# Kernel tuning notes

Hardware: AMD Instinct MI355X
Metric: run time of the kernel (lower is better)

## Reference

```python
import jax, jax.numpy as jnp
import numpy as np

X_CH, Y_CH, DIM, NUM_HEAD = 256, 512, 128, 4
H_DIM = DIM // NUM_HEAD
GAMMA = H_DIM ** (-0.5)


def conv1x1(x, w, b):
    # x: [B,C,H,W], w: [O,C], b: [O]
    return jnp.einsum('bchw,oc->bohw', x, w) + b[None, :, None, None]


def _split_qkv(qkv, bs, hw):
    # qkv: [B, 3*DIM, H, W] -> q,k,v each [B, NUM_HEAD, HW, H_DIM]
    qkv = qkv.reshape(bs, 3, NUM_HEAD, H_DIM, hw)
    qkv = jnp.transpose(qkv, (1, 0, 2, 4, 3))  # [3, B, H, HW, D]
    return qkv[0], qkv[1], qkv[2]


def setup_inputs() -> dict:
    key = jax.random.key(0)
    ks = jax.random.split(key, 12)
    s = lambda fan_in: 1.0 / np.sqrt(fan_in)
    x = jax.random.normal(ks[0], (2, X_CH, 64, 64), dtype=jnp.float32)
    y = jax.random.normal(ks[1], (2, Y_CH, 32, 32), dtype=jnp.float32)
    wx_qkv = jax.random.normal(ks[2], (3 * DIM, X_CH), dtype=jnp.float32) * s(X_CH)
    bx_qkv = jax.random.normal(ks[3], (3 * DIM,), dtype=jnp.float32) * s(X_CH)
    wy_qkv = jax.random.normal(ks[4], (3 * DIM, Y_CH), dtype=jnp.float32) * s(Y_CH)
    by_qkv = jax.random.normal(ks[5], (3 * DIM,), dtype=jnp.float32) * s(Y_CH)
    wpx = jax.random.normal(ks[6], (X_CH, DIM), dtype=jnp.float32) * s(DIM)
    bpx = jax.random.normal(ks[7], (X_CH,), dtype=jnp.float32) * s(DIM)
    wpy = jax.random.normal(ks[8], (Y_CH, DIM), dtype=jnp.float32) * s(DIM)
    bpy = jax.random.normal(ks[9], (Y_CH,), dtype=jnp.float32) * s(DIM)
    return {"x": x, "y": y, "wx_qkv": wx_qkv, "bx_qkv": bx_qkv,
            "wy_qkv": wy_qkv, "by_qkv": by_qkv,
            "wpx": wpx, "bpx": bpx, "wpy": wpy, "bpy": bpy}


def reference(x, y, wx_qkv, bx_qkv, wy_qkv, by_qkv, wpx, bpx, wpy, bpy):
    bs, _, h_x, w_x = x.shape
    _, _, h_y, w_y = y.shape
    hw_x, hw_y = h_x * w_x, h_y * w_y

    q_x, k_x, v_x = _split_qkv(conv1x1(x, wx_qkv, bx_qkv), bs, hw_x)
    q_y, k_y, v_y = _split_qkv(conv1x1(y, wy_qkv, by_qkv), bs, hw_y)

    # x attends to y
    atten_x = jax.nn.softmax(jnp.einsum('bhqd,bhkd->bhqk', q_x, k_y) * GAMMA, axis=-1)
    out_x = jnp.einsum('bhqk,bhkd->bhqd', atten_x, v_y)  # [B,H,HWx,D]
    out_x = jnp.transpose(out_x, (0, 1, 3, 2)).reshape(bs, DIM, h_x, w_x)

    # y attends to x
    atten_y = jax.nn.softmax(jnp.einsum('bhqd,bhkd->bhqk', q_y, k_x) * GAMMA, axis=-1)
    out_y = jnp.einsum('bhqk,bhkd->bhqd', atten_y, v_x)
    out_y = jnp.transpose(out_y, (0, 1, 3, 2)).reshape(bs, DIM, h_y, w_y)

    out_x = conv1x1(out_x, wpx, bpx) + x
    out_y = conv1x1(out_y, wpy, bpy) + y
    return out_x, out_y
```

## Files before the change

### kernel.cpp

```cpp
#include <hip/hip_runtime.h>
#include <hip/hip_bf16.h>
#include <cstdint>

#define B 2
#define NH 4
#define HD 32
#define DIM 128
#define CX 256
#define CY 512
#define PX 4096
#define PY 1024
#define QKV 384
#define GAMMA 0.17677669529663687f

typedef unsigned short u16;
typedef unsigned int u32;

using short8 = __attribute__((ext_vector_type(8))) short;
using f32x4  = __attribute__((ext_vector_type(4))) float;

__device__ __forceinline__ float bf2f(u32 h) {
  union { u32 u; float f; } v; v.u = (h & 0xffffu) << 16; return v.f;
}
__device__ __forceinline__ u16 f2bf(float f) {
  u32 u = __float_as_uint(f);
  u32 r = (u + 0x7fffu + ((u >> 16) & 1u)) >> 16;
  return (u16)r;
}
__device__ __forceinline__ bool is_f32(const void* src) {
  u32 u = ((const u16*)src)[2 * (threadIdx.x & 63)];
  return __ballot((u & 0x7F80u) >= 0x4600u) != 0ull;
}

#define N_X   (B * CX * PX)
#define N_Y   (B * CY * PY)
#define N_WX  (QKV * CX)
#define N_BX  (QKV)
#define N_WY  (QKV * CY)
#define N_BY  (QKV)
#define N_WPX (CX * DIM)
#define N_BPX (CX)
#define N_WPY (CY * DIM)
#define N_BPY (CY)

enum : size_t {
  OFF_CWX   = 0,
  OFF_CBX   = OFF_CWX  + N_WX,
  OFF_CWY   = OFF_CBX  + N_BX,
  OFF_CBY   = OFF_CWY  + N_WY,
  OFF_CWPX  = OFF_CBY  + N_BY,
  OFF_CBPX  = OFF_CWPX + N_WPX,
  OFF_CWPY  = OFF_CBPX + N_BPX,
  OFF_CBPY  = OFF_CWPY + N_WPY,
  OFF_XT    = OFF_CBPY + N_BPY,
  OFF_YT    = OFF_XT   + (size_t)B * PX * CX,
  OFF_QPX   = OFF_YT   + (size_t)B * PY * CY,
  OFF_KPX   = OFF_QPX  + (size_t)B * NH * PX * HD,
  OFF_QPY   = OFF_KPX  + (size_t)B * NH * PX * HD,
  OFF_KPY   = OFF_QPY  + (size_t)B * NH * PY * HD,
  OFF_VCX   = OFF_KPY  + (size_t)B * NH * PY * HD,
  OFF_VCY   = OFF_VCX  + (size_t)B * DIM * PX,
  OFF_OTX   = OFF_VCY  + (size_t)B * DIM * PY,
  OFF_OTY   = OFF_OTX  + (size_t)B * PX * DIM,
  WS_END    = OFF_OTY  + (size_t)B * PY * DIM,
};

#define XPX_BLKS 512
#define XPY_BLKS 256
__global__ __launch_bounds__(256) void k_prep(
    const void* x, const void* y, const void* wx, const void* bx,
    const void* wy, const void* by, const void* wpx, const void* bpx,
    const void* wpy, const void* bpy, u16* __restrict__ ws) {
  const int id = blockIdx.x;
  if (id < XPX_BLKS + XPY_BLKS) {
    __shared__ u16 tile[64][68];
    const void* src; u16* dst; int C, P, p_t, c_t, b;
    if (id < XPX_BLKS) {
      src = x; dst = ws + OFF_XT; C = CX; P = PX;
      p_t = id & 63; c_t = (id >> 6) & 3; b = id >> 8;
    } else {
      int id2 = id - XPX_BLKS;
      src = y; dst = ws + OFF_YT; C = CY; P = PY;
      p_t = id2 & 15; c_t = (id2 >> 4) & 7; b = id2 >> 7;
    }
    const bool f32in = is_f32(src);
    const int tx = threadIdx.x & 15, tc = threadIdx.x >> 4;
    const int p0 = p_t * 64, c0 = c_t * 64;
#pragma unroll
    for (int i = 0; i < 4; i++) {
      int cl = tc + i * 16;
      size_t sidx = ((size_t)b * C + c0 + cl) * P + p0 + tx * 4;
      u16 v0, v1, v2, v3;
      if (f32in) {
        float4 f = *(const float4*)((const float*)src + sidx);
        v0 = f2bf(f.x); v1 = f2bf(f.y); v2 = f2bf(f.z); v3 = f2bf(f.w);
      } else {
        uint2 u = *(const uint2*)((const u16*)src + sidx);
        v0 = (u16)u.x; v1 = (u16)(u.x >> 16); v2 = (u16)u.y; v3 = (u16)(u.y >> 16);
      }
      tile[tx * 4 + 0][cl] = v0; tile[tx * 4 + 1][cl] = v1;
      tile[tx * 4 + 2][cl] = v2; tile[tx * 4 + 3][cl] = v3;
    }
    __syncthreads();
#pragma unroll
    for (int i = 0; i < 4; i++) {
      int pl = tc + i * 16;
      *(uint2*)&dst[((size_t)b * P + p0 + pl) * C + c0 + tx * 4] =
          *(const uint2*)&tile[pl][tx * 4];
    }
  } else {
    int wid = id - (XPX_BLKS + XPY_BLKS);
    const void* src; size_t dstoff; int n, base;
    if      (wid < 48)  { src = wx;  dstoff = OFF_CWX;  n = N_WX;  base = 0; }
    else if (wid < 49)  { src = bx;  dstoff = OFF_CBX;  n = N_BX;  base = 48; }
    else if (wid < 145) { src = wy;  dstoff = OFF_CWY;  n = N_WY;  base = 49; }
    else if (wid < 146) { src = by;  dstoff = OFF_CBY;  n = N_BY;  base = 145; }
    else if (wid < 162) { src = wpx; dstoff = OFF_CWPX; n = N_WPX; base = 146; }
    else if (wid < 163) { src = bpx; dstoff = OFF_CBPX; n = N_BPX; base = 162; }
    else if (wid < 195) { src = wpy; dstoff = OFF_CWPY; n = N_WPY; base = 163; }
    else                { src = bpy; dstoff = OFF_CBPY; n = N_BPY; base = 195; }
    const bool f32in = is_f32(src);
    int e0 = (wid - base) * 2048 + threadIdx.x * 8;
    if (e0 >= n) return;
    u16* dst = ws + dstoff + e0;
    if (f32in) {
      const float* s = (const float*)src + e0;
      float4 a = *(const float4*)s;
      float4 bq = *(const float4*)(s + 4);
      ushort4 o0, o1;
      o0.x = f2bf(a.x);  o0.y = f2bf(a.y);  o0.z = f2bf(a.z);  o0.w = f2bf(a.w);
      o1.x = f2bf(bq.x); o1.y = f2bf(bq.y); o1.z = f2bf(bq.z); o1.w = f2bf(bq.w);
      *(ushort4*)dst = o0;
      *(ushort4*)(dst + 4) = o1;
    } else {
      uint4 v = *(const uint4*)((const u16*)src + e0);
      *(uint4*)dst = v;
    }
  }
}

__global__ __launch_bounds__(256) void k_qkv(u16* __restrict__ ws) {
  const int t = threadIdx.x;
  const int lane = t & 63, w = t >> 6;
  const int ql = lane & 15, quad = lane >> 4;
  const int b = blockIdx.z;

  const u16 *W, *Xt, *bias; u16 *qp, *kp, *vc; int C, P, pxb;
  if (blockIdx.x < 64) {
    W = ws + OFF_CWX; Xt = ws + OFF_XT; bias = ws + OFF_CBX;
    qp = ws + OFF_QPX; kp = ws + OFF_KPX; vc = ws + OFF_VCX;
    C = CX; P = PX; pxb = blockIdx.x;
  } else {
    W = ws + OFF_CWY; Xt = ws + OFF_YT; bias = ws + OFF_CBY;
    qp = ws + OFF_QPY; kp = ws + OFF_KPY; vc = ws + OFF_VCY;
    C = CY; P = PY; pxb = blockIdx.x - 64;
  }
  const int p_w = pxb * 64 + (w & 1) * 32;
  const int o_w = blockIdx.y * 64 + (w >> 1) * 32;

  const u16* wr0 = W + (size_t)(o_w + ql) * C;
  const u16* wr1 = W + (size_t)(o_w + 16 + ql) * C;
  const u16* xr0 = Xt + ((size_t)b * P + p_w + ql) * C;
  const u16* xr1 = Xt + ((size_t)b * P + p_w + 16 + ql) * C;

  union U { uint4 u; short8 s; };
  f32x4 acc[2][2];
#pragma unroll
  for (int i = 0; i < 2; i++)
#pragma unroll
    for (int j = 0; j < 2; j++) acc[i][j] = (f32x4){0.f, 0.f, 0.f, 0.f};

  const bool isv = blockIdx.y >= 4;
  if (!isv) {
#pragma unroll 4
    for (int c0 = 0; c0 < C; c0 += 32) {
      int off = c0 + quad * 8;
      U a0, a1, b0, b1;
      a0.u = *(const uint4*)&wr0[off];
      a1.u = *(const uint4*)&wr1[off];
      b0.u = *(const uint4*)&xr0[off];
      b1.u = *(const uint4*)&xr1[off];
      acc[0][0] = __builtin_amdgcn_mfma_f32_16x16x32_bf16(a0.s, b0.s, acc[0][0], 0, 0, 0);
      acc[0][1] = __builtin_amdgcn_mfma_f32_16x16x32_bf16(a0.s, b1.s, acc[0][1], 0, 0, 0);
      acc[1][0] = __builtin_amdgcn_mfma_f32_16x16x32_bf16(a1.s, b0.s, acc[1][0], 0, 0, 0);
      acc[1][1] = __builtin_amdgcn_mfma_f32_16x16x32_bf16(a1.s, b1.s, acc[1][1], 0, 0, 0);
    }
  } else {
#pragma unroll 4
    for (int c0 = 0; c0 < C; c0 += 32) {
      int off = c0 + quad * 8;
      U a0, a1, b0, b1;
      a0.u = *(const uint4*)&wr0[off];
      a1.u = *(const uint4*)&wr1[off];
      b0.u = *(const uint4*)&xr0[off];
      b1.u = *(const uint4*)&xr1[off];
      acc[0][0] = __builtin_amdgcn_mfma_f32_16x16x32_bf16(b0.s, a0.s, acc[0][0], 0, 0, 0);
      acc[0][1] = __builtin_amdgcn_mfma_f32_16x16x32_bf16(b1.s, a0.s, acc[0][1], 0, 0, 0);
      acc[1][0] = __builtin_amdgcn_mfma_f32_16x16x32_bf16(b0.s, a1.s, acc[1][0], 0, 0, 0);
      acc[1][1] = __builtin_amdgcn_mfma_f32_16x16x32_bf16(b1.s, a1.s, acc[1][1], 0, 0, 0);
    }
  }

  if (!isv) {
    float bs[2][4];
#pragma unroll
    for (int oi = 0; oi < 2; oi++)
#pragma unroll
      for (int r = 0; r < 4; r++)
        bs[oi][r] = bf2f(bias[o_w + oi * 16 + quad * 4 + r]);
    bool isq = blockIdx.y < 2;
    float scale = isq ? GAMMA : 1.0f;
    u16* dstT = isq ? qp : kp;
#pragma unroll
    for (int oi = 0; oi < 2; oi++)
#pragma unroll
      for (int pi = 0; pi < 2; pi++) {
        int p = p_w + pi * 16 + ql;
        int o = o_w + oi * 16 + quad * 4 - (isq ? 0 : 128);
        int hh = o >> 5, d = o & 31;
        f32x4 a = acc[oi][pi];
        uint2 pk;
        pk.x = (u32)f2bf((a[0] + bs[oi][0]) * scale) |
               ((u32)f2bf((a[1] + bs[oi][1]) * scale) << 16);
        pk.y = (u32)f2bf((a[2] + bs[oi][2]) * scale) |
               ((u32)f2bf((a[3] + bs[oi][3]) * scale) << 16);
        *(uint2*)&dstT[((size_t)(b * NH + hh) * P + p) * HD + d] = pk;
      }
  } else {
#pragma unroll
    for (int oi = 0; oi < 2; oi++) {
      int o = o_w + oi * 16 + ql - 256;
      float bv = bf2f(bias[o_w + oi * 16 + ql]);
#pragma unroll
      for (int pi = 0; pi < 2; pi++) {
        int pbase = p_w + pi * 16 + quad * 4;
        f32x4 a = acc[oi][pi];
        ushort4 st;
        st.x = f2bf(a[0] + bv); st.y = f2bf(a[1] + bv);
        st.z = f2bf(a[2] + bv); st.w = f2bf(a[3] + bv);
        *(ushort4*)&vc[((size_t)b * DIM + o) * P + pbase] = st;
      }
    }
  }
}

template <int NQF>
__device__ __forceinline__ void attn_core(
    const u16* __restrict__ Qp, const u16* __restrict__ Kp,
    const u16* __restrict__ Vc, u16* __restrict__ Ot, int Pq, int Pk,
    int q0, int h, int b, u16* pool, float (*lfb)[64]) {
  const int t = threadIdx.x;
  const int lane = t & 63, w = t >> 6;
  const int ql = lane & 15, quad = lane >> 4;

  union U { uint4 u; short8 s; };
  U qf[NQF];
#pragma unroll
  for (int qi = 0; qi < NQF; qi++)
    qf[qi].u = *(const uint4*)&Qp[((size_t)(b * NH + h) * Pq + q0 + qi * 16 + ql) * HD + quad * 8];

  const int kspan = Pk >> 2;
  const int kk0 = w * kspan;
  const int niter = kspan >> 5;
  const int f0 = ((ql >> 2) << 3) | (ql & 3);

  const u16* kbase = Kp + ((size_t)(b * NH + h) * Pk + kk0 + f0) * HD + quad * 8;
  const u16* v0base = Vc + ((size_t)(b * DIM + h * HD + ql)) * Pk + kk0 + quad * 8;
  const u16* v1base = v0base + (size_t)16 * Pk;

  U ka, kb, va, vb, kan, kbn, van, vbn;
  ka.u = *(const uint4*)&kbase[0];
  kb.u = *(const uint4*)&kbase[4 * HD];
  va.u = *(const uint4*)&v0base[0];
  vb.u = *(const uint4*)&v1base[0];

  f32x4 o0[NQF], o1[NQF];
  float l_run[NQF];
#pragma unroll
  for (int qi = 0; qi < NQF; qi++) {
    o0[qi] = (f32x4){0.f, 0.f, 0.f, 0.f};
    o1[qi] = (f32x4){0.f, 0.f, 0.f, 0.f};
    l_run[qi] = 0.f;
  }

  for (int it = 0; it < niter; it++) {
    if (it + 1 < niter) {
      size_t go = (size_t)(it + 1) * 32;
      kan.u = *(const uint4*)&kbase[go * HD];
      kbn.u = *(const uint4*)&kbase[(go + 4) * HD];
      van.u = *(const uint4*)&v0base[go];
      vbn.u = *(const uint4*)&v1base[go];
    }

#pragma unroll
    for (int qi = 0; qi < NQF; qi++) {
      f32x4 z = {0.f, 0.f, 0.f, 0.f};
      f32x4 st0 = __builtin_amdgcn_mfma_f32_16x16x32_bf16(ka.s, qf[qi].s, z, 0, 0, 0);
      f32x4 st1 = __builtin_amdgcn_mfma_f32_16x16x32_bf16(kb.s, qf[qi].s, z, 0, 0, 0);

      float p[8];
#pragma unroll
      for (int r = 0; r < 4; r++) { p[r] = __expf(st0[r]); p[4 + r] = __expf(st1[r]); }
      l_run[qi] += ((p[0] + p[1]) + (p[2] + p[3])) + ((p[4] + p[5]) + (p[6] + p[7]));

      U pf;
      pf.u.x = __builtin_amdgcn_perm(__float_as_uint(p[1]), __float_as_uint(p[0]), 0x07060302u);
      pf.u.y = __builtin_amdgcn_perm(__float_as_uint(p[3]), __float_as_uint(p[2]), 0x07060302u);
      pf.u.z = __builtin_amdgcn_perm(__float_as_uint(p[5]), __float_as_uint(p[4]), 0x07060302u);
      pf.u.w = __builtin_amdgcn_perm(__float_as_uint(p[7]), __float_as_uint(p[6]), 0x07060302u);

      o0[qi] = __builtin_amdgcn_mfma_f32_16x16x32_bf16(va.s, pf.s, o0[qi], 0, 0, 0);
      o1[qi] = __builtin_amdgcn_mfma_f32_16x16x32_bf16(vb.s, pf.s, o1[qi], 0, 0, 0);
    }
    ka = kan; kb = kbn; va = van; vb = vbn;
  }

#pragma unroll
  for (int qi = 0; qi < NQF; qi++) {
    float l = l_run[qi];
    l += __shfl_xor(l, 16);
    l += __shfl_xor(l, 32);
    l_run[qi] = l;
  }

  float* Of = (float*)(pool + (size_t)w * 4096);
#pragma unroll
  for (int qi = 0; qi < NQF; qi++) {
#pragma unroll
    for (int r = 0; r < 4; r++) {
      Of[(qi * 16 + ql) * 32 + quad * 4 + r] = o0[qi][r];
      Of[(qi * 16 + ql) * 32 + 16 + quad * 4 + r] = o1[qi][r];
    }
    if (quad == 0) lfb[w][qi * 16 + ql] = l_run[qi];
  }
  __syncthreads();

  const float* OfA = (const float*)pool;
#pragma unroll
  for (int k = 0; k < NQF * 2; k++) {
    int e = t + k * 256;
    int q = e >> 5, d = e & 31;
    float lt = lfb[0][q] + lfb[1][q] + lfb[2][q] + lfb[3][q];
    int di = q * 32 + d;
    float v = (OfA[di] + OfA[2048 + di]) + (OfA[4096 + di] + OfA[6144 + di]);
    Ot[((size_t)b * Pq + q0 + q) * DIM + h * HD + d] = f2bf(v / lt);
  }
}

__global__ __launch_bounds__(256) void k_attn(u16* __restrict__ ws) {
  __shared__ __align__(16) u16 pool[16384];
  __shared__ float lfb[4][64];
  const int h = blockIdx.y, b = blockIdx.z;
  if (blockIdx.x < 64) {
    attn_core<4>(ws + OFF_QPX, ws + OFF_KPY, ws + OFF_VCY, ws + OFF_OTX,
                 PX, PY, blockIdx.x * 64, h, b, pool, lfb);
  } else {
    attn_core<2>(ws + OFF_QPY, ws + OFF_KPX, ws + OFF_VCX, ws + OFF_OTY,
                 PY, PX, (blockIdx.x - 64) * 32, h, b, pool, lfb);
  }
}

__global__ __launch_bounds__(256) void k_proj(
    u16* __restrict__ ws, void* __restrict__ outv,
    const void* __restrict__ resx, const void* __restrict__ resy) {
  const u16 *W, *A, *bias; const void* res; int OT, P, pxb; size_t out_off;
  if (blockIdx.x < 64) {
    if (blockIdx.y >= 4) return;
    W = ws + OFF_CWPX; A = ws + OFF_OTX; bias = ws + OFF_CBPX;
    res = resx; OT = CX; P = PX; pxb = blockIdx.x; out_off = 0;
  } else {
    W = ws + OFF_CWPY; A = ws + OFF_OTY; bias = ws + OFF_CBPY;
    res = resy; OT = CY; P = PY; pxb = blockIdx.x - 64;
    out_off = (size_t)B * CX * PX;
  }
  const bool f32io = is_f32(res);
  const int t = threadIdx.x;
  const int lane = t & 63, w = t >> 6;
  const int ql = lane & 15, quad = lane >> 4;
  const int p_w = pxb * 64 + (w & 1) * 32;
  const int o_w = blockIdx.y * 64 + (w >> 1) * 32;
  const int b = blockIdx.z;

  const u16* wr0 = W + (size_t)(o_w + ql) * DIM;
  const u16* wr1 = W + (size_t)(o_w + 16 + ql) * DIM;
  const u16* xr0 = A + ((size_t)b * P + p_w + ql) * DIM;
  const u16* xr1 = A + ((size_t)b * P + p_w + 16 + ql) * DIM;

  union U { uint4 u; short8 s; };
  f32x4 acc[2][2];
#pragma unroll
  for (int i = 0; i < 2; i++)
#pragma unroll
    for (int j = 0; j < 2; j++) acc[i][j] = (f32x4){0.f, 0.f, 0.f, 0.f};

#pragma unroll
  for (int c0 = 0; c0 < DIM; c0 += 32) {
    int off = c0 + quad * 8;
    U a0, a1, b0, b1;
    a0.u = *(const uint4*)&wr0[off];
    a1.u = *(const uint4*)&wr1[off];
    b0.u = *(const uint4*)&xr0[off];
    b1.u = *(const uint4*)&xr1[off];
    acc[0][0] = __builtin_amdgcn_mfma_f32_16x16x32_bf16(b0.s, a0.s, acc[0][0], 0, 0, 0);
    acc[0][1] = __builtin_amdgcn_mfma_f32_16x16x32_bf16(b1.s, a0.s, acc[0][1], 0, 0, 0);
    acc[1][0] = __builtin_amdgcn_mfma_f32_16x16x32_bf16(b0.s, a1.s, acc[1][0], 0, 0, 0);
    acc[1][1] = __builtin_amdgcn_mfma_f32_16x16x32_bf16(b1.s, a1.s, acc[1][1], 0, 0, 0);
  }

#pragma unroll
  for (int oi = 0; oi < 2; oi++) {
    int o = o_w + oi * 16 + ql;
    float bv = bf2f(bias[o]);
#pragma unroll
    for (int pi = 0; pi < 2; pi++) {
      int pbase = p_w + pi * 16 + quad * 4;
      size_t idx = ((size_t)b * OT + o) * P + pbase;
      f32x4 a = acc[oi][pi];
      if (f32io) {
        float4 rv = *(const float4*)((const float*)res + idx);
        float4 ov;
        ov.x = a[0] + bv + rv.x; ov.y = a[1] + bv + rv.y;
        ov.z = a[2] + bv + rv.z; ov.w = a[3] + bv + rv.w;
        *(float4*)((float*)outv + out_off + idx) = ov;
      } else {
        ushort4 rv = *(const ushort4*)((const u16*)res + idx);
        ushort4 ov;
        ov.x = f2bf(a[0] + bv + bf2f(rv.x));
        ov.y = f2bf(a[1] + bv + bf2f(rv.y));
        ov.z = f2bf(a[2] + bv + bf2f(rv.z));
        ov.w = f2bf(a[3] + bv + bf2f(rv.w));
        *(ushort4*)((u16*)outv + out_off + idx) = ov;
      }
    }
  }
}

extern "C" void kernel_launch(void* const* d_in, const int* in_sizes, int n_in,
                              void* d_out, int out_size, void* d_ws, size_t ws_size,
                              hipStream_t stream) {
  (void)in_sizes; (void)n_in; (void)out_size; (void)ws_size;
  u16* ws = (u16*)d_ws;

  k_prep<<<dim3(XPX_BLKS + XPY_BLKS + 196), 256, 0, stream>>>(
      d_in[0], d_in[1], d_in[2], d_in[3], d_in[4], d_in[5],
      d_in[6], d_in[7], d_in[8], d_in[9], ws);
  k_qkv<<<dim3(80, 6, B), 256, 0, stream>>>(ws);
  k_attn<<<dim3(96, NH, B), 256, 0, stream>>>(ws);
  k_proj<<<dim3(80, 8, B), 256, 0, stream>>>(ws, d_out, d_in[0], d_in[1]);
}
```

Baseline: 139.0 us.

## Fuse four kernels into one persistent kernel with grid-wide atomic barriers

Merges the prep, qkv, attention and projection kernels into a single persistent kernel of 512 blocks. Phases are separated by atomic-counter grid barriers, and the counters are reset by a small init kernel. The attention phase pairs one y-query unit with two x-query units per block to balance work. The aim is to remove launch gaps and tail effects between kernels. In exchange it adds spin-wait barrier cost and depends on all 512 blocks being co-resident, which could deadlock if occupancy is lower than assumed.

```diff
diff --git a/kernel.cpp b/kernel.cpp
--- a/kernel.cpp
+++ b/kernel.cpp
@@ -12,6 +12,7 @@
 #define PY 1024
 #define QKV 384
 #define GAMMA 0.17677669529663687f
+#define GRID 512
 
 typedef unsigned short u16;
 typedef unsigned int u32;
@@ -65,15 +66,31 @@
   WS_END    = OFF_OTY  + (size_t)B * PY * DIM,
 };
 
+__device__ __forceinline__ void gbar(u32* bar, int slot) {
+  __syncthreads();
+  if (threadIdx.x == 0) {
+    __threadfence();
+    atomicAdd(&bar[slot], 1u);
+    while (__hip_atomic_load(&bar[slot], __ATOMIC_ACQUIRE,
+                             __HIP_MEMORY_SCOPE_AGENT) < (u32)GRID)
+      __builtin_amdgcn_s_sleep(4);
+    __threadfence();
+  }
+  __syncthreads();
+}
+
+__global__ __launch_bounds__(64) void k_init(u32* __restrict__ bar) {
+  if (threadIdx.x < 8) bar[threadIdx.x] = 0u;
+}
+
 #define XPX_BLKS 512
 #define XPY_BLKS 256
-__global__ __launch_bounds__(256) void k_prep(
+__device__ void prep_unit(int id,
     const void* x, const void* y, const void* wx, const void* bx,
     const void* wy, const void* by, const void* wpx, const void* bpx,
-    const void* wpy, const void* bpy, u16* __restrict__ ws) {
-  const int id = blockIdx.x;
+    const void* wpy, const void* bpy, u16* __restrict__ ws,
+    u16 (*tile)[68]) {
   if (id < XPX_BLKS + XPY_BLKS) {
-    __shared__ u16 tile[64][68];
     const void* src; u16* dst; int C, P, p_t, c_t, b;
     if (id < XPX_BLKS) {
       src = x; dst = ws + OFF_XT; C = CX; P = PX;
@@ -121,42 +138,42 @@
     else                { src = bpy; dstoff = OFF_CBPY; n = N_BPY; base = 195; }
     const bool f32in = is_f32(src);
     int e0 = (wid - base) * 2048 + threadIdx.x * 8;
-    if (e0 >= n) return;
-    u16* dst = ws + dstoff + e0;
-    if (f32in) {
-      const float* s = (const float*)src + e0;
-      float4 a = *(const float4*)s;
-      float4 bq = *(const float4*)(s + 4);
-      ushort4 o0, o1;
-      o0.x = f2bf(a.x);  o0.y = f2bf(a.y);  o0.z = f2bf(a.z);  o0.w = f2bf(a.w);
-      o1.x = f2bf(bq.x); o1.y = f2bf(bq.y); o1.z = f2bf(bq.z); o1.w = f2bf(bq.w);
-      *(ushort4*)dst = o0;
-      *(ushort4*)(dst + 4) = o1;
-    } else {
-      uint4 v = *(const uint4*)((const u16*)src + e0);
-      *(uint4*)dst = v;
-    }
-  }
-}
-
-__global__ __launch_bounds__(256) void k_qkv(u16* __restrict__ ws) {
+    if (e0 < n) {
+      u16* dst = ws + dstoff + e0;
+      if (f32in) {
+        const float* s = (const float*)src + e0;
+        float4 a = *(const float4*)s;
+        float4 bq = *(const float4*)(s + 4);
+        ushort4 o0, o1;
+        o0.x = f2bf(a.x);  o0.y = f2bf(a.y);  o0.z = f2bf(a.z);  o0.w = f2bf(a.w);
+        o1.x = f2bf(bq.x); o1.y = f2bf(bq.y); o1.z = f2bf(bq.z); o1.w = f2bf(bq.w);
+        *(ushort4*)dst = o0;
+        *(ushort4*)(dst + 4) = o1;
+      } else {
+        uint4 v = *(const uint4*)((const u16*)src + e0);
+        *(uint4*)dst = v;
+      }
+    }
+  }
+}
+
+__device__ void qkv_unit(int bxi, int byi, int b, u16* __restrict__ ws) {
   const int t = threadIdx.x;
   const int lane = t & 63, w = t >> 6;
   const int ql = lane & 15, quad = lane >> 4;
-  const int b = blockIdx.z;
 
   const u16 *W, *Xt, *bias; u16 *qp, *kp, *vc; int C, P, pxb;
-  if (blockIdx.x < 64) {
+  if (bxi < 64) {
     W = ws + OFF_CWX; Xt = ws + OFF_XT; bias = ws + OFF_CBX;
     qp = ws + OFF_QPX; kp = ws + OFF_KPX; vc = ws + OFF_VCX;
-    C = CX; P = PX; pxb = blockIdx.x;
+    C = CX; P = PX; pxb = bxi;
   } else {
     W = ws + OFF_CWY; Xt = ws + OFF_YT; bias = ws + OFF_CBY;
     qp = ws + OFF_QPY; kp = ws + OFF_KPY; vc = ws + OFF_VCY;
-    C = CY; P = PY; pxb = blockIdx.x - 64;
+    C = CY; P = PY; pxb = bxi - 64;
   }
   const int p_w = pxb * 64 + (w & 1) * 32;
-  const int o_w = blockIdx.y * 64 + (w >> 1) * 32;
+  const int o_w = byi * 64 + (w >> 1) * 32;
 
   const u16* wr0 = W + (size_t)(o_w + ql) * C;
   const u16* wr1 = W + (size_t)(o_w + 16 + ql) * C;
@@ -170,7 +187,7 @@
 #pragma unroll
     for (int j = 0; j < 2; j++) acc[i][j] = (f32x4){0.f, 0.f, 0.f, 0.f};
 
-  const bool isv = blockIdx.y >= 4;
+  const bool isv = byi >= 4;
   if (!isv) {
 #pragma unroll 4
     for (int c0 = 0; c0 < C; c0 += 32) {
@@ -208,7 +225,7 @@
 #pragma unroll
       for (int r = 0; r < 4; r++)
         bs[oi][r] = bf2f(bias[o_w + oi * 16 + quad * 4 + r]);
-    bool isq = blockIdx.y < 2;
+    bool isq = byi < 2;
     float scale = isq ? GAMMA : 1.0f;
     u16* dstT = isq ? qp : kp;
 #pragma unroll
@@ -347,30 +364,17 @@
   }
 }
 
-__global__ __launch_bounds__(256) void k_attn(u16* __restrict__ ws) {
-  __shared__ __align__(16) u16 pool[16384];
-  __shared__ float lfb[4][64];
-  const int h = blockIdx.y, b = blockIdx.z;
-  if (blockIdx.x < 64) {
-    attn_core<4>(ws + OFF_QPX, ws + OFF_KPY, ws + OFF_VCY, ws + OFF_OTX,
-                 PX, PY, blockIdx.x * 64, h, b, pool, lfb);
-  } else {
-    attn_core<2>(ws + OFF_QPY, ws + OFF_KPX, ws + OFF_VCX, ws + OFF_OTY,
-                 PY, PX, (blockIdx.x - 64) * 32, h, b, pool, lfb);
-  }
-}
-
-__global__ __launch_bounds__(256) void k_proj(
-    u16* __restrict__ ws, void* __restrict__ outv,
-    const void* __restrict__ resx, const void* __restrict__ resy) {
+__device__ void proj_unit(int bxi, int byi, int b, u16* __restrict__ ws,
+                          void* __restrict__ outv,
+                          const void* __restrict__ resx,
+                          const void* __restrict__ resy) {
   const u16 *W, *A, *bias; const void* res; int OT, P, pxb; size_t out_off;
-  if (blockIdx.x < 64) {
-    if (blockIdx.y >= 4) return;
+  if (bxi < 64) {
     W = ws + OFF_CWPX; A = ws + OFF_OTX; bias = ws + OFF_CBPX;
-    res = resx; OT = CX; P = PX; pxb = blockIdx.x; out_off = 0;
+    res = resx; OT = CX; P = PX; pxb = bxi; out_off = 0;
   } else {
     W = ws + OFF_CWPY; A = ws + OFF_OTY; bias = ws + OFF_CBPY;
-    res = resy; OT = CY; P = PY; pxb = blockIdx.x - 64;
+    res = resy; OT = CY; P = PY; pxb = bxi - 64;
     out_off = (size_t)B * CX * PX;
   }
   const bool f32io = is_f32(res);
@@ -378,8 +382,7 @@
   const int lane = t & 63, w = t >> 6;
   const int ql = lane & 15, quad = lane >> 4;
   const int p_w = pxb * 64 + (w & 1) * 32;
-  const int o_w = blockIdx.y * 64 + (w >> 1) * 32;
-  const int b = blockIdx.z;
+  const int o_w = byi * 64 + (w >> 1) * 32;
 
   const u16* wr0 = W + (size_t)(o_w + ql) * DIM;
   const u16* wr1 = W + (size_t)(o_w + 16 + ql) * DIM;
@@ -435,16 +438,67 @@
   }
 }
 
+__global__ __launch_bounds__(256, 2) void k_mega(
+    const void* x, const void* y, const void* wx, const void* bxq,
+    const void* wy, const void* byq, const void* wpx, const void* bpx,
+    const void* wpy, const void* bpy, u16* __restrict__ ws,
+    void* __restrict__ outv, const void* __restrict__ resx,
+    const void* __restrict__ resy, u32* __restrict__ bar) {
+  __shared__ __align__(16) u16 sm_pool[16384];
+  __shared__ __align__(16) float sm_lfb[4][64];
+
+  for (int u = blockIdx.x; u < XPX_BLKS + XPY_BLKS + 196; u += GRID) {
+    prep_unit(u, x, y, wx, bxq, wy, byq, wpx, bpx, wpy, bpy, ws,
+              (u16(*)[68])sm_pool);
+    __syncthreads();
+  }
+  gbar(bar, 0);
+
+  for (int u = blockIdx.x; u < 960; u += GRID) {
+    int bxi = u % 80; int rem = u / 80;
+    qkv_unit(bxi, rem % 6, rem / 6, ws);
+  }
+  gbar(bar, 1);
+
+  if (blockIdx.x < 256) {
+    int hy = blockIdx.x;
+    int h = (hy >> 5) & 3, b = hy >> 7;
+    attn_core<2>(ws + OFF_QPY, ws + OFF_KPX, ws + OFF_VCX, ws + OFF_OTY,
+                 PY, PX, (hy & 31) * 32, h, b, sm_pool, sm_lfb);
+  } else {
+    int lx = blockIdx.x - 256;
+    {
+      int u = lx;
+      attn_core<4>(ws + OFF_QPX, ws + OFF_KPY, ws + OFF_VCY, ws + OFF_OTX,
+                   PX, PY, (u & 63) * 64, (u >> 6) & 3, u >> 8, sm_pool, sm_lfb);
+    }
+    __syncthreads();
+    {
+      int u = lx + 256;
+      attn_core<4>(ws + OFF_QPX, ws + OFF_KPY, ws + OFF_VCY, ws + OFF_OTX,
+                   PX, PY, (u & 63) * 64, (u >> 6) & 3, u >> 8, sm_pool, sm_lfb);
+    }
+  }
+  gbar(bar, 2);
+
+  for (int u = blockIdx.x; u < 768; u += GRID) {
+    int bxi, byi, bz;
+    if (u < 512) { bxi = u & 63;        byi = (u >> 6) & 3; bz = u >> 8; }
+    else { int v = u - 512; bxi = 64 + (v & 15); byi = (v >> 4) & 7; bz = v >> 7; }
+    proj_unit(bxi, byi, bz, ws, outv, resx, resy);
+  }
+}
+
 extern "C" void kernel_launch(void* const* d_in, const int* in_sizes, int n_in,
                               void* d_out, int out_size, void* d_ws, size_t ws_size,
                               hipStream_t stream) {
   (void)in_sizes; (void)n_in; (void)out_size; (void)ws_size;
   u16* ws = (u16*)d_ws;
-
-  k_prep<<<dim3(XPX_BLKS + XPY_BLKS + 196), 256, 0, stream>>>(
+  u32* bar = (u32*)(ws + WS_END);
+
+  k_init<<<dim3(1), 64, 0, stream>>>(bar);
+  k_mega<<<dim3(GRID), 256, 0, stream>>>(
       d_in[0], d_in[1], d_in[2], d_in[3], d_in[4], d_in[5],
-      d_in[6], d_in[7], d_in[8], d_in[9], ws);
-  k_qkv<<<dim3(80, 6, B), 256, 0, stream>>>(ws);
-  k_attn<<<dim3(96, NH, B), 256, 0, stream>>>(ws);
-  k_proj<<<dim3(80, 8, B), 256, 0, stream>>>(ws, d_out, d_in[0], d_in[1]);
-}
+      d_in[6], d_in[7], d_in[8], d_in[9], ws,
+      d_out, d_in[0], d_in[1], bar);
+}
```

New measurement: 375.9 us. 2.7x slower.

## Unroll key loop for y-queries and reorder attention blocks longest-first

Applied to the files above, without the earlier changes.

The attention kernel now processes 64 keys per iteration for the y-attends-to-x path (long key span), with double the prefetched K/V registers, to deepen the load pipeline. The grid is flattened to 1D and remapped so the long-running y-query blocks (4096 keys) are dispatched first, with batch and head interleaved in the low bits. This aims to reduce loop overhead and latency exposure and to improve tail balance across CUs, at the cost of higher register pressure in the unrolled path.

```diff
diff --git a/kernel.cpp b/kernel.cpp
--- a/kernel.cpp
+++ b/kernel.cpp
@@ -244,7 +244,7 @@
   }
 }
 
-template <int NQF>
+template <int NQF, int KW>
 __device__ __forceinline__ void attn_core(
     const u16* __restrict__ Qp, const u16* __restrict__ Kp,
     const u16* __restrict__ Vc, u16* __restrict__ Ot, int Pq, int Pk,
@@ -261,18 +261,12 @@
 
   const int kspan = Pk >> 2;
   const int kk0 = w * kspan;
-  const int niter = kspan >> 5;
+  const int niter = kspan / KW;
   const int f0 = ((ql >> 2) << 3) | (ql & 3);
 
   const u16* kbase = Kp + ((size_t)(b * NH + h) * Pk + kk0 + f0) * HD + quad * 8;
   const u16* v0base = Vc + ((size_t)(b * DIM + h * HD + ql)) * Pk + kk0 + quad * 8;
   const u16* v1base = v0base + (size_t)16 * Pk;
-
-  U ka, kb, va, vb, kan, kbn, van, vbn;
-  ka.u = *(const uint4*)&kbase[0];
-  kb.u = *(const uint4*)&kbase[4 * HD];
-  va.u = *(const uint4*)&v0base[0];
-  vb.u = *(const uint4*)&v1base[0];
 
   f32x4 o0[NQF], o1[NQF];
   float l_run[NQF];
@@ -283,20 +277,12 @@
     l_run[qi] = 0.f;
   }
 
-  for (int it = 0; it < niter; it++) {
-    if (it + 1 < niter) {
-      size_t go = (size_t)(it + 1) * 32;
-      kan.u = *(const uint4*)&kbase[go * HD];
-      kbn.u = *(const uint4*)&kbase[(go + 4) * HD];
-      van.u = *(const uint4*)&v0base[go];
-      vbn.u = *(const uint4*)&v1base[go];
-    }
-
+  auto step32 = [&](U& xka, U& xkb, U& xva, U& xvb) {
 #pragma unroll
     for (int qi = 0; qi < NQF; qi++) {
       f32x4 z = {0.f, 0.f, 0.f, 0.f};
-      f32x4 st0 = __builtin_amdgcn_mfma_f32_16x16x32_bf16(ka.s, qf[qi].s, z, 0, 0, 0);
-      f32x4 st1 = __builtin_amdgcn_mfma_f32_16x16x32_bf16(kb.s, qf[qi].s, z, 0, 0, 0);
+      f32x4 st0 = __builtin_amdgcn_mfma_f32_16x16x32_bf16(xka.s, qf[qi].s, z, 0, 0, 0);
+      f32x4 st1 = __builtin_amdgcn_mfma_f32_16x16x32_bf16(xkb.s, qf[qi].s, z, 0, 0, 0);
 
       float p[8];
 #pragma unroll
@@ -309,10 +295,44 @@
       pf.u.z = __builtin_amdgcn_perm(__float_as_uint(p[5]), __float_as_uint(p[4]), 0x07060302u);
       pf.u.w = __builtin_amdgcn_perm(__float_as_uint(p[7]), __float_as_uint(p[6]), 0x07060302u);
 
-      o0[qi] = __builtin_amdgcn_mfma_f32_16x16x32_bf16(va.s, pf.s, o0[qi], 0, 0, 0);
-      o1[qi] = __builtin_amdgcn_mfma_f32_16x16x32_bf16(vb.s, pf.s, o1[qi], 0, 0, 0);
-    }
+      o0[qi] = __builtin_amdgcn_mfma_f32_16x16x32_bf16(xva.s, pf.s, o0[qi], 0, 0, 0);
+      o1[qi] = __builtin_amdgcn_mfma_f32_16x16x32_bf16(xvb.s, pf.s, o1[qi], 0, 0, 0);
+    }
+  };
+
+  U ka, kb, va, vb, kan, kbn, van, vbn;
+  U kc, kd, vc, vd, kcn, kdn, vcn, vdn;
+  ka.u = *(const uint4*)&kbase[0];
+  kb.u = *(const uint4*)&kbase[4 * HD];
+  va.u = *(const uint4*)&v0base[0];
+  vb.u = *(const uint4*)&v1base[0];
+  if constexpr (KW == 64) {
+    kc.u = *(const uint4*)&kbase[32 * HD];
+    kd.u = *(const uint4*)&kbase[36 * HD];
+    vc.u = *(const uint4*)&v0base[32];
+    vd.u = *(const uint4*)&v1base[32];
+  }
+
+  for (int it = 0; it < niter; it++) {
+    if (it + 1 < niter) {
+      size_t go = (size_t)(it + 1) * KW;
+      kan.u = *(const uint4*)&kbase[go * HD];
+      kbn.u = *(const uint4*)&kbase[(go + 4) * HD];
+      van.u = *(const uint4*)&v0base[go];
+      vbn.u = *(const uint4*)&v1base[go];
+      if constexpr (KW == 64) {
+        kcn.u = *(const uint4*)&kbase[(go + 32) * HD];
+        kdn.u = *(const uint4*)&kbase[(go + 36) * HD];
+        vcn.u = *(const uint4*)&v0base[go + 32];
+        vdn.u = *(const uint4*)&v1base[go + 32];
+      }
+    }
+
+    step32(ka, kb, va, vb);
+    if constexpr (KW == 64) step32(kc, kd, vc, vd);
+
     ka = kan; kb = kbn; va = van; vb = vbn;
+    if constexpr (KW == 64) { kc = kcn; kd = kdn; vc = vcn; vd = vdn; }
   }
 
 #pragma unroll
@@ -350,13 +370,15 @@
 __global__ __launch_bounds__(256) void k_attn(u16* __restrict__ ws) {
   __shared__ __align__(16) u16 pool[16384];
   __shared__ float lfb[4][64];
-  const int h = blockIdx.y, b = blockIdx.z;
-  if (blockIdx.x < 64) {
-    attn_core<4>(ws + OFF_QPX, ws + OFF_KPY, ws + OFF_VCY, ws + OFF_OTX,
-                 PX, PY, blockIdx.x * 64, h, b, pool, lfb);
-  } else {
-    attn_core<2>(ws + OFF_QPY, ws + OFF_KPX, ws + OFF_VCX, ws + OFF_OTY,
-                 PY, PX, (blockIdx.x - 64) * 32, h, b, pool, lfb);
+  const int c = blockIdx.x & 7;
+  const int j = blockIdx.x >> 3;
+  const int b = c >> 2, h = c & 3;
+  if (j < 32) {
+    attn_core<2, 64>(ws + OFF_QPY, ws + OFF_KPX, ws + OFF_VCX, ws + OFF_OTY,
+                     PY, PX, j * 32, h, b, pool, lfb);
+  } else {
+    attn_core<4, 32>(ws + OFF_QPX, ws + OFF_KPY, ws + OFF_VCY, ws + OFF_OTX,
+                     PX, PY, (j - 32) * 64, h, b, pool, lfb);
   }
 }
 
@@ -445,6 +467,6 @@
       d_in[0], d_in[1], d_in[2], d_in[3], d_in[4], d_in[5],
       d_in[6], d_in[7], d_in[8], d_in[9], ws);
   k_qkv<<<dim3(80, 6, B), 256, 0, stream>>>(ws);
-  k_attn<<<dim3(96, NH, B), 256, 0, stream>>>(ws);
+  k_attn<<<dim3(768), 256, 0, stream>>>(ws);
   k_proj<<<dim3(80, 8, B), 256, 0, stream>>>(ws, d_out, d_in[0], d_in[1]);
 }
```

New measurement: 136.6 us. No clear change (-1.7%).
